# Performance work log

Measured on AMD Instinct MI355X. Metric: run time of the kernel, lower is better.

The kernel has to match this reference:

```python
import jax, jax.numpy as jnp
import numpy as np

EMBED = 1024
HEADS = 16
HEAD_DIM = EMBED // HEADS
N, SEQ = 4, 2048


def setup_inputs() -> dict:
    key = jax.random.key(0)
    ks = jax.random.split(key, 9)
    values = jax.random.normal(ks[0], (N, SEQ, EMBED), dtype=jnp.float32)
    keys = jax.random.normal(ks[1], (N, SEQ, EMBED), dtype=jnp.float32)
    query = jax.random.normal(ks[2], (N, SEQ, EMBED), dtype=jnp.float32)
    mask = jax.random.randint(ks[3], (N, 1, SEQ, SEQ), 0, 2, dtype=jnp.int32)
    s_h = 1.0 / np.sqrt(HEAD_DIM)
    s_e = 1.0 / np.sqrt(EMBED)
    Wv = jax.random.normal(ks[4], (HEAD_DIM, HEAD_DIM), dtype=jnp.float32) * s_h
    Wk = jax.random.normal(ks[5], (HEAD_DIM, HEAD_DIM), dtype=jnp.float32) * s_h
    Wq = jax.random.normal(ks[6], (HEAD_DIM, HEAD_DIM), dtype=jnp.float32) * s_h
    Wo = jax.random.normal(ks[7], (EMBED, EMBED), dtype=jnp.float32) * s_e
    bo = jax.random.normal(ks[8], (EMBED,), dtype=jnp.float32) * 0.01
    return {"values": values, "keys": keys, "query": query, "mask": mask,
            "Wv": Wv, "Wk": Wk, "Wq": Wq, "Wo": Wo, "bo": bo}


def reference(values, keys, query, mask, Wv, Wk, Wq, Wo, bo):
    n, q_len = query.shape[0], query.shape[1]
    k_len, v_len = keys.shape[1], values.shape[1]
    # split heads: [N, L, H, D]
    v = values.reshape(n, v_len, HEADS, HEAD_DIM)
    k = keys.reshape(n, k_len, HEADS, HEAD_DIM)
    q = query.reshape(n, q_len, HEADS, HEAD_DIM)
    # per-head linear projections (nn.Linear: x @ W.T)
    v = jnp.einsum('nlhd,ed->nlhe', v, Wv)
    k = jnp.einsum('nlhd,ed->nlhe', k, Wk)
    q = jnp.einsum('nlhd,ed->nlhe', q, Wq)
    # [N, H, Q, K] scores
    energy = jnp.einsum('nqhd,nkhd->nhqk', q, k)
    energy = jnp.where(mask == 0, jnp.float32(-1e20), energy)
    # note: original scales by sqrt(embed_size), not sqrt(head_dim)
    attention = jax.nn.softmax(energy / jnp.sqrt(jnp.float32(EMBED)), axis=3)
    out = jnp.einsum('nhql,nlhd->nqhd', attention, v).reshape(n, q_len, EMBED)
    return out @ Wo.T + bo
```

## Files before the change

kernel.cpp:

```cpp
#include <hip/hip_runtime.h>
#include <hip/hip_bf16.h>

typedef __attribute__((ext_vector_type(8))) short bfx8;
typedef __attribute__((ext_vector_type(4))) float fx4;
typedef __attribute__((ext_vector_type(16))) float f32x16;
typedef __attribute__((ext_vector_type(4))) unsigned u32x4;

#define MFMA16(a,b,c) __builtin_amdgcn_mfma_f32_16x16x32_bf16((a),(b),(c),0,0,0)
#define MFMA32(a,b,c) __builtin_amdgcn_mfma_f32_32x32x16_bf16((a),(b),(c),0,0,0)

__device__ __forceinline__ unsigned short bfc(float x){
  return __builtin_bit_cast(unsigned short, __float2bfloat16(x));
}
__device__ __forceinline__ unsigned pack2(float a, float b){
  return (unsigned)bfc(a) | ((unsigned)bfc(b) << 16);
}
__device__ __forceinline__ bfx8 cvt8(const float* p){
  const float4* q = (const float4*)p;
  float4 a = q[0], b = q[1];
  bfx8 r;
  r[0]=(short)bfc(a.x); r[1]=(short)bfc(a.y); r[2]=(short)bfc(a.z); r[3]=(short)bfc(a.w);
  r[4]=(short)bfc(b.x); r[5]=(short)bfc(b.y); r[6]=(short)bfc(b.z); r[7]=(short)bfc(b.w);
  return r;
}
__device__ __forceinline__ void g2l16(const void* g, void* l){
  __builtin_amdgcn_global_load_lds((const __attribute__((address_space(1))) unsigned*)g,
                                   (__attribute__((address_space(3))) unsigned*)l, 16, 0, 0);
}
__device__ __forceinline__ float mexp(float zv, unsigned mws, int pos){
  float e = __builtin_amdgcn_exp2f(zv);
  unsigned msk = (unsigned)(((int)(mws << (31-pos))) >> 31);
  return __builtin_bit_cast(float, __builtin_bit_cast(unsigned, e) & msk);
}
__device__ __forceinline__ f32x16 zero16(){
  f32x16 z;
  #pragma unroll
  for (int i=0;i<16;++i) z[i] = 0.f;
  return z;
}

#define SCL 0.04508422002778f

__global__ __launch_bounds__(256) void prep_k(const float* __restrict__ Xv, const float* __restrict__ Xk,
                                              const float* __restrict__ Xq,
                                              const float* __restrict__ Wv, const float* __restrict__ Wk,
                                              const float* __restrict__ Wq,
                                              const int* __restrict__ M, const float* __restrict__ Wo,
                                              unsigned short* __restrict__ Vt, unsigned short* __restrict__ Kb,
                                              unsigned short* __restrict__ Qb,
                                              unsigned long long* __restrict__ mT,
                                              unsigned short* __restrict__ Wob){
  int bid = blockIdx.x;
  int tid = threadIdx.x, l = tid & 63, wv = tid >> 6, g = l >> 4, j = l & 15;
  if (bid >= 3072){
    int pid = bid - 3072;
    if (pid < 1024){
      int task = pid*4 + wv;
      int n = task >> 10, rem = task & 1023, kt = rem >> 5, qc = rem & 31;
      int qbase = qc*64;
      const int* mp = M + (size_t)n*2048*2048 + (size_t)kt*64 + l;
      unsigned long long myw = 0;
      for (int qq = 0; qq < 64; ++qq){
        unsigned long long b = __ballot(mp[(size_t)(qbase+qq)*2048] != 0);
        if (l == qq) myw = b;
      }
      mT[((size_t)n*32 + kt)*2048 + qbase + l] = myw;
    } else {
      int i = ((pid-1024)*256 + tid)*8;
      bfx8 v = cvt8(Wo + i);
      *(bfx8*)(Wob + i) = v;
    }
    return;
  }
  int which = bid >> 10;
  int r = bid & 1023;
  int nh = r >> 4, sb = r & 15;
  int n = nh >> 4, h = nh & 15;
  const float* X = (which==0) ? Xv : ((which==1) ? Xk : Xq);
  const float* W = (which==0) ? Wv : ((which==1) ? Wk : Wq);
  int s0 = sb*128 + wv*32;
  size_t xbase = (size_t)n*2048*1024 + (size_t)h*64;

  if (which){
    float sc = (which==2) ? SCL : 1.0f;
    bfx8 bw[4][2];
    for (int nt=0;nt<4;++nt) for (int ks=0;ks<2;++ks)
      bw[nt][ks] = cvt8(W + (nt*16 + j)*64 + ks*32 + g*8);
    bfx8 ax[2][2];
    for (int mt=0;mt<2;++mt){
      const float* xp = X + xbase + (size_t)(s0 + mt*16 + j)*1024;
      for (int ks=0;ks<2;++ks) ax[mt][ks] = cvt8(xp + ks*32 + g*8);
    }
    fx4 acc[2][4];
    for (int mt=0;mt<2;++mt) for (int nt=0;nt<4;++nt) acc[mt][nt] = (fx4){0.f,0.f,0.f,0.f};
    for (int mt=0;mt<2;++mt) for (int nt=0;nt<4;++nt) for (int ks=0;ks<2;++ks)
      acc[mt][nt] = MFMA16(ax[mt][ks], bw[nt][ks], acc[mt][nt]);
    unsigned short* O = ((which==1) ? Kb : Qb) + (size_t)nh*2048*64;
    for (int mt=0;mt<2;++mt) for (int nt=0;nt<4;++nt) for (int rr=0;rr<4;++rr){
      int s = s0 + mt*16 + g*4 + rr, e = nt*16 + j;
      O[(size_t)s*64 + e] = bfc(acc[mt][nt][rr]*sc);
    }
  } else {
    bfx8 aw[4][2];
    for (int mt=0;mt<4;++mt) for (int ks=0;ks<2;++ks)
      aw[mt][ks] = cvt8(W + (mt*16 + j)*64 + ks*32 + g*8);
    bfx8 bx[2][2];
    for (int nt=0;nt<2;++nt){
      const float* xp = X + xbase + (size_t)(s0 + nt*16 + j)*1024;
      for (int ks=0;ks<2;++ks) bx[nt][ks] = cvt8(xp + ks*32 + g*8);
    }
    fx4 acc[4][2];
    for (int mt=0;mt<4;++mt) for (int nt=0;nt<2;++nt) acc[mt][nt] = (fx4){0.f,0.f,0.f,0.f};
    for (int mt=0;mt<4;++mt) for (int nt=0;nt<2;++nt) for (int ks=0;ks<2;++ks)
      acc[mt][nt] = MFMA16(aw[mt][ks], bx[nt][ks], acc[mt][nt]);
    unsigned short* O = Vt + (size_t)nh*64*2048;
    for (int mt=0;mt<4;++mt) for (int nt=0;nt<2;++nt) for (int rr=0;rr<4;++rr){
      int d = mt*16 + g*4 + rr, s = s0 + nt*16 + j;
      O[(size_t)d*2048 + s] = bfc(acc[mt][nt][rr]);
    }
  }
}

__global__ __launch_bounds__(512, 4) void flash_k(const unsigned short* __restrict__ Qb,
                                                  const unsigned short* __restrict__ Kb,
                                                  const unsigned short* __restrict__ Vt,
                                                  const unsigned long long* __restrict__ mT,
                                                  unsigned short* __restrict__ AO){
  __shared__ short lK[2][64*64];
  __shared__ short lV[2][64*64];
  int tid = threadIdx.x;
  int l = tid & 63, wv = tid >> 6, hi = l >> 5, c = l & 31;
  int cl7 = c & 7, hi4 = hi*4;
  int bid = blockIdx.x;
  int nh = bid >> 3, qb = bid & 7;
  int n = nh >> 4, h = nh & 15;
  const unsigned short* Qp = Qb + (size_t)nh*131072;
  const unsigned short* Kp = Kb + (size_t)nh*131072;
  const unsigned short* Vp = Vt + (size_t)nh*131072;
  int q = qb*256 + wv*32 + c;
  bfx8 qf[4];
  #pragma unroll
  for (int s=0;s<4;++s) qf[s] = *(const bfx8*)(Qp + (size_t)q*64 + s*16 + hi*8);
  f32x16 accO0 = zero16(), accO1 = zero16();
  float ls = 0.f;
  const unsigned long long* mrow = mT + (size_t)n*65536 + q;
  int rowK0 = c*128;
  int rowK1 = rowK0 + 4096;

  int sidx = wv*64 + l;
  int srow = sidx >> 3, scs = (sidx & 7) ^ (srow & 7);
  const unsigned short* Ksrc = Kp + (size_t)srow*64 + scs*8;
  const unsigned short* Vsrc = Vp + (size_t)srow*2048 + scs*8;

  g2l16(Ksrc, (char*)lK[0] + sidx*16);
  g2l16(Vsrc, (char*)lV[0] + sidx*16);
  __syncthreads();

#define PROC_TILE(zz, mws, TT, VB) do { \
    unsigned Wt[8]; \
    _Pragma("unroll") \
    for (int wi=0; wi<8; ++wi){ \
      const int r0 = 2*wi; \
      const int pos = (r0&3) + 8*(r0>>2); \
      float p0_ = mexp((zz)[r0],   (mws), pos); \
      float p1_ = mexp((zz)[r0+1], (mws), pos+1); \
      ls += p0_ + p1_; \
      Wt[wi] = pack2(p0_, p1_); \
    } \
    _Pragma("unroll") \
    for (int mm=0; mm<2; ++mm){ \
      unsigned xa = hi ? Wt[4*mm+0] : Wt[4*mm+2]; \
      unsigned xb = hi ? Wt[4*mm+1] : Wt[4*mm+3]; \
      unsigned ra = (unsigned)__shfl_xor((int)xa, 32); \
      unsigned rb = (unsigned)__shfl_xor((int)xb, 32); \
      u32x4 pw; \
      pw.x = hi ? ra : Wt[4*mm+0]; \
      pw.y = hi ? rb : Wt[4*mm+1]; \
      pw.z = hi ? Wt[4*mm+2] : ra; \
      pw.w = hi ? Wt[4*mm+3] : rb; \
      bfx8 pb = __builtin_bit_cast(bfx8, pw); \
      const int ch2 = 2*((TT)*2+mm); \
      bfx8 vf0 = *(const bfx8*)((VB) + rowK0 + (((ch2+hi) ^ cl7) << 4)); \
      bfx8 vf1 = *(const bfx8*)((VB) + rowK1 + (((ch2+hi) ^ cl7) << 4)); \
      accO0 = MFMA32(vf0, pb, accO0); \
      accO1 = MFMA32(vf1, pb, accO1); \
    } \
  } while(0)

#define ATTN_ITER(BUF, NBUF, kt) do { \
    if ((kt) < 31){ \
      g2l16(Ksrc + (size_t)((kt)+1)*4096, (char*)lK[NBUF] + sidx*16); \
      g2l16(Vsrc + (size_t)((kt)+1)*64,   (char*)lV[NBUF] + sidx*16); \
    } \
    unsigned long long mw = mrow[(size_t)(kt)*2048]; \
    const char* KB = (const char*)lK[BUF]; \
    const char* VB = (const char*)lV[BUF]; \
    f32x16 z0 = zero16(), z1 = zero16(); \
    _Pragma("unroll") \
    for (int s=0; s<4; ++s){ \
      bfx8 kf0 = *(const bfx8*)(KB + rowK0 + (((2*s+hi) ^ cl7) << 4)); \
      bfx8 kf1 = *(const bfx8*)(KB + rowK1 + (((2*s+hi) ^ cl7) << 4)); \
      z0 = MFMA32(kf0, qf[s], z0); \
      z1 = MFMA32(kf1, qf[s], z1); \
    } \
    unsigned mws0 = ((unsigned)mw) >> hi4; \
    unsigned mws1 = ((unsigned)(mw >> 32)) >> hi4; \
    PROC_TILE(z0, mws0, 0, VB); \
    PROC_TILE(z1, mws1, 1, VB); \
    __syncthreads(); \
  } while(0)

  #pragma unroll 1
  for (int kt2 = 0; kt2 < 32; kt2 += 2){
    ATTN_ITER(0, 1, kt2);
    ATTN_ITER(1, 0, kt2+1);
  }
#undef ATTN_ITER
#undef PROC_TILE

  ls += __shfl_xor(ls, 32);
  float inv = 1.0f / ls;
  unsigned short* aop = AO + ((size_t)n*2048 + q)*1024 + h*64;
  #pragma unroll
  for (int u=0; u<4; ++u){
    int d0 = u*8 + hi4;
    ushort4 o;
    o.x = bfc(accO0[4*u+0]*inv); o.y = bfc(accO0[4*u+1]*inv);
    o.z = bfc(accO0[4*u+2]*inv); o.w = bfc(accO0[4*u+3]*inv);
    *(ushort4*)(aop + d0) = o;
    ushort4 o1;
    o1.x = bfc(accO1[4*u+0]*inv); o1.y = bfc(accO1[4*u+1]*inv);
    o1.z = bfc(accO1[4*u+2]*inv); o1.w = bfc(accO1[4*u+3]*inv);
    *(ushort4*)(aop + 32 + d0) = o1;
  }
}

__global__ __launch_bounds__(256) void gemm_k(const unsigned short* __restrict__ AO,
                                              const unsigned short* __restrict__ Wob,
                                              const float* __restrict__ bo, float* __restrict__ out){
  __shared__ short lA[2][128*32], lB[2][128*32];
  int tid = threadIdx.x, l = tid & 63, wv = tid >> 6, g = l >> 4, j = l & 15;
  int wr = wv >> 1, wc = wv & 1;
  int bid = blockIdx.x;
  int m0 = (bid >> 3)*128, n0 = (bid & 7)*128;
  fx4 acc[4][4];
  #pragma unroll
  for (int mt=0;mt<4;++mt) for (int nt=0;nt<4;++nt) acc[mt][nt] = (fx4){0.f,0.f,0.f,0.f};

  int sbase = wv*128;
  int sidx0 = sbase + l, sidx1 = sbase + 64 + l;
  int srow0 = sidx0 >> 2, sc0 = sidx0 & 3;
  int srow1 = sidx1 >> 2, sc1 = sidx1 & 3;
  const unsigned short* Asrc0 = AO  + (size_t)(m0+srow0)*1024 + sc0*8;
  const unsigned short* Asrc1 = AO  + (size_t)(m0+srow1)*1024 + sc1*8;
  const unsigned short* Bsrc0 = Wob + (size_t)(n0+srow0)*1024 + sc0*8;
  const unsigned short* Bsrc1 = Wob + (size_t)(n0+srow1)*1024 + sc1*8;

  #define GSTAGE(b, kb) do { \
    g2l16(Asrc0 + (kb)*32, (char*)lA[b] + sidx0*16); \
    g2l16(Asrc1 + (kb)*32, (char*)lA[b] + sidx1*16); \
    g2l16(Bsrc0 + (kb)*32, (char*)lB[b] + sidx0*16); \
    g2l16(Bsrc1 + (kb)*32, (char*)lB[b] + sidx1*16); \
  } while(0)

  GSTAGE(0, 0);
  __syncthreads();
  int b = 0;
  for (int kb = 0; kb < 32; ++kb){
    if (kb < 31) GSTAGE(b^1, kb+1);
    bfx8 af[4], bfr[4];
    #pragma unroll
    for (int mt=0;mt<4;++mt) af[mt]  = *(const bfx8*)((const char*)lA[b] + (wr*64 + mt*16 + j)*64 + g*16);
    #pragma unroll
    for (int nt=0;nt<4;++nt) bfr[nt] = *(const bfx8*)((const char*)lB[b] + (wc*64 + nt*16 + j)*64 + g*16);
    #pragma unroll
    for (int mt=0;mt<4;++mt)
      #pragma unroll
      for (int nt=0;nt<4;++nt)
        acc[mt][nt] = MFMA16(af[mt], bfr[nt], acc[mt][nt]);
    __syncthreads();
    b ^= 1;
  }
  #undef GSTAGE

  #pragma unroll
  for (int mt=0;mt<4;++mt)
    #pragma unroll
    for (int nt=0;nt<4;++nt){
      int mm = m0 + wr*64 + mt*16 + g*4;
      int oo = n0 + wc*64 + nt*16 + j;
      float bb = bo[oo];
      #pragma unroll
      for (int rr=0;rr<4;++rr)
        out[(size_t)(mm+rr)*1024 + oo] = acc[mt][nt][rr] + bb;
    }
}

extern "C" void kernel_launch(void* const* d_in, const int* in_sizes, int n_in,
                              void* d_out, int out_size, void* d_ws, size_t ws_size,
                              hipStream_t stream){
  const float* V  = (const float*)d_in[0];
  const float* K  = (const float*)d_in[1];
  const float* Q  = (const float*)d_in[2];
  const int*   M  = (const int*)d_in[3];
  const float* Wv = (const float*)d_in[4];
  const float* Wk = (const float*)d_in[5];
  const float* Wq = (const float*)d_in[6];
  const float* Wo = (const float*)d_in[7];
  const float* bo = (const float*)d_in[8];

  char* ws = (char*)d_ws;
  unsigned short* Qb = (unsigned short*)(ws + ((size_t)0  << 20));
  unsigned short* Kb = (unsigned short*)(ws + ((size_t)16 << 20));
  unsigned short* Vt = (unsigned short*)(ws + ((size_t)32 << 20));
  unsigned short* AO = (unsigned short*)(ws + ((size_t)48 << 20));
  unsigned long long* mT = (unsigned long long*)(ws + ((size_t)64 << 20));
  unsigned short* Wob = (unsigned short*)(ws + ((size_t)66 << 20));

  hipLaunchKernelGGL(prep_k,  dim3(4608), dim3(256), 0, stream,
                     V, K, Q, Wv, Wk, Wq, M, Wo, Vt, Kb, Qb, mT, Wob);
  hipLaunchKernelGGL(flash_k, dim3(512),  dim3(512), 0, stream, Qb, Kb, Vt, mT, AO);
  hipLaunchKernelGGL(gemm_k,  dim3(512),  dim3(256), 0, stream, AO, Wob, bo, (float*)d_out);
}
```

Baseline: 192.8 us.

## Use 32x32x8 MFMA for PV to drop shuffles; smaller blocks, remapped grid

The PV product now uses the 32x32x8 bf16 MFMA, so each lane's packed P values feed the B operand directly and the cross-half __shfl_xor exchange goes away. The attention kernel also changes from 512 threads covering 256 queries to 256 threads covering 128 queries per block, with twice as many blocks and a blockIdx remap that interleaves heads. Each thread now stages two 16-byte chunks per tile, the LDS XOR swizzle gains a second term to cut bank conflicts, and the mask word is prefetched one tile ahead. In exchange, PV issues twice as many MFMAs at half the K depth, and K/V tiles are loaded into LDS by twice as many blocks.

```diff
diff --git a/kernel.cpp b/kernel.cpp
--- a/kernel.cpp
+++ b/kernel.cpp
@@ -2,12 +2,21 @@
 #include <hip/hip_bf16.h>
 
 typedef __attribute__((ext_vector_type(8))) short bfx8;
+typedef __attribute__((ext_vector_type(4))) short bfx4;
 typedef __attribute__((ext_vector_type(4))) float fx4;
 typedef __attribute__((ext_vector_type(16))) float f32x16;
-typedef __attribute__((ext_vector_type(4))) unsigned u32x4;
 
 #define MFMA16(a,b,c) __builtin_amdgcn_mfma_f32_16x16x32_bf16((a),(b),(c),0,0,0)
 #define MFMA32(a,b,c) __builtin_amdgcn_mfma_f32_32x32x16_bf16((a),(b),(c),0,0,0)
+
+__device__ __forceinline__ f32x16 mfma32x8(bfx4 a, bfx4 b, f32x16 c){
+#if __has_builtin(__builtin_amdgcn_mfma_f32_32x32x8bf16_1k)
+  return __builtin_amdgcn_mfma_f32_32x32x8bf16_1k(a, b, c, 0, 0, 0);
+#else
+  asm("v_mfma_f32_32x32x8_bf16 %0, %1, %2, %0" : "+v"(c) : "v"(a), "v"(b));
+  return c;
+#endif
+}
 
 __device__ __forceinline__ unsigned short bfc(float x){
   return __builtin_bit_cast(unsigned short, __float2bfloat16(x));
@@ -121,7 +130,7 @@
   }
 }
 
-__global__ __launch_bounds__(512, 4) void flash_k(const unsigned short* __restrict__ Qb,
+__global__ __launch_bounds__(256, 4) void flash_k(const unsigned short* __restrict__ Qb,
                                                   const unsigned short* __restrict__ Kb,
                                                   const unsigned short* __restrict__ Vt,
                                                   const unsigned long long* __restrict__ mT,
@@ -130,14 +139,16 @@
   __shared__ short lV[2][64*64];
   int tid = threadIdx.x;
   int l = tid & 63, wv = tid >> 6, hi = l >> 5, c = l & 31;
-  int cl7 = c & 7, hi4 = hi*4;
-  int bid = blockIdx.x;
-  int nh = bid >> 3, qb = bid & 7;
+  int swc = (c & 7) ^ ((c >> 3) & 3);
+  int hi4 = hi*4;
+  int bid0 = blockIdx.x;
+  int bid = (bid0 & 7)*128 + (bid0 >> 3);
+  int nh = bid >> 4, qb = bid & 15;
   int n = nh >> 4, h = nh & 15;
   const unsigned short* Qp = Qb + (size_t)nh*131072;
   const unsigned short* Kp = Kb + (size_t)nh*131072;
   const unsigned short* Vp = Vt + (size_t)nh*131072;
-  int q = qb*256 + wv*32 + c;
+  int q = qb*128 + wv*32 + c;
   bfx8 qf[4];
   #pragma unroll
   for (int s=0;s<4;++s) qf[s] = *(const bfx8*)(Qp + (size_t)q*64 + s*16 + hi*8);
@@ -147,14 +158,24 @@
   int rowK0 = c*128;
   int rowK1 = rowK0 + 4096;
 
-  int sidx = wv*64 + l;
-  int srow = sidx >> 3, scs = (sidx & 7) ^ (srow & 7);
-  const unsigned short* Ksrc = Kp + (size_t)srow*64 + scs*8;
-  const unsigned short* Vsrc = Vp + (size_t)srow*2048 + scs*8;
-
-  g2l16(Ksrc, (char*)lK[0] + sidx*16);
-  g2l16(Vsrc, (char*)lV[0] + sidx*16);
+  int sidx0 = wv*64 + l, sidx1 = sidx0 + 256;
+  int srow0 = sidx0 >> 3, scs0 = (sidx0 & 7) ^ (srow0 & 7) ^ ((srow0 >> 3) & 3);
+  int srow1 = sidx1 >> 3, scs1 = (sidx1 & 7) ^ (srow1 & 7) ^ ((srow1 >> 3) & 3);
+  const unsigned short* Ksrc0 = Kp + (size_t)srow0*64 + scs0*8;
+  const unsigned short* Ksrc1 = Kp + (size_t)srow1*64 + scs1*8;
+  const unsigned short* Vsrc0 = Vp + (size_t)srow0*2048 + scs0*8;
+  const unsigned short* Vsrc1 = Vp + (size_t)srow1*2048 + scs1*8;
+
+  #define STAGE(b, kt) do { \
+    g2l16(Ksrc0 + (size_t)(kt)*4096, (char*)lK[b] + sidx0*16); \
+    g2l16(Ksrc1 + (size_t)(kt)*4096, (char*)lK[b] + sidx1*16); \
+    g2l16(Vsrc0 + (size_t)(kt)*64,   (char*)lV[b] + sidx0*16); \
+    g2l16(Vsrc1 + (size_t)(kt)*64,   (char*)lV[b] + sidx1*16); \
+  } while(0)
+
+  STAGE(0, 0);
   __syncthreads();
+  unsigned long long mwcur = mrow[0];
 
 #define PROC_TILE(zz, mws, TT, VB) do { \
     unsigned Wt[8]; \
@@ -168,38 +189,28 @@
       Wt[wi] = pack2(p0_, p1_); \
     } \
     _Pragma("unroll") \
-    for (int mm=0; mm<2; ++mm){ \
-      unsigned xa = hi ? Wt[4*mm+0] : Wt[4*mm+2]; \
-      unsigned xb = hi ? Wt[4*mm+1] : Wt[4*mm+3]; \
-      unsigned ra = (unsigned)__shfl_xor((int)xa, 32); \
-      unsigned rb = (unsigned)__shfl_xor((int)xb, 32); \
-      u32x4 pw; \
-      pw.x = hi ? ra : Wt[4*mm+0]; \
-      pw.y = hi ? rb : Wt[4*mm+1]; \
-      pw.z = hi ? Wt[4*mm+2] : ra; \
-      pw.w = hi ? Wt[4*mm+3] : rb; \
-      bfx8 pb = __builtin_bit_cast(bfx8, pw); \
-      const int ch2 = 2*((TT)*2+mm); \
-      bfx8 vf0 = *(const bfx8*)((VB) + rowK0 + (((ch2+hi) ^ cl7) << 4)); \
-      bfx8 vf1 = *(const bfx8*)((VB) + rowK1 + (((ch2+hi) ^ cl7) << 4)); \
-      accO0 = MFMA32(vf0, pb, accO0); \
-      accO1 = MFMA32(vf1, pb, accO1); \
+    for (int wl=0; wl<4; ++wl){ \
+      const int w = 4*(TT) + wl; \
+      uint2 u2; u2.x = Wt[2*wl]; u2.y = Wt[2*wl+1]; \
+      bfx4 pb = __builtin_bit_cast(bfx4, u2); \
+      bfx4 vf0 = *(const bfx4*)((VB) + rowK0 + (((w ^ swc) << 4) + hi*8)); \
+      bfx4 vf1 = *(const bfx4*)((VB) + rowK1 + (((w ^ swc) << 4) + hi*8)); \
+      accO0 = mfma32x8(vf0, pb, accO0); \
+      accO1 = mfma32x8(vf1, pb, accO1); \
     } \
   } while(0)
 
 #define ATTN_ITER(BUF, NBUF, kt) do { \
-    if ((kt) < 31){ \
-      g2l16(Ksrc + (size_t)((kt)+1)*4096, (char*)lK[NBUF] + sidx*16); \
-      g2l16(Vsrc + (size_t)((kt)+1)*64,   (char*)lV[NBUF] + sidx*16); \
-    } \
-    unsigned long long mw = mrow[(size_t)(kt)*2048]; \
+    if ((kt) < 31) STAGE(NBUF, (kt)+1); \
+    unsigned long long mw = mwcur; \
+    mwcur = mrow[(size_t)((kt)+1 < 32 ? (kt)+1 : 31)*2048]; \
     const char* KB = (const char*)lK[BUF]; \
     const char* VB = (const char*)lV[BUF]; \
     f32x16 z0 = zero16(), z1 = zero16(); \
     _Pragma("unroll") \
     for (int s=0; s<4; ++s){ \
-      bfx8 kf0 = *(const bfx8*)(KB + rowK0 + (((2*s+hi) ^ cl7) << 4)); \
-      bfx8 kf1 = *(const bfx8*)(KB + rowK1 + (((2*s+hi) ^ cl7) << 4)); \
+      bfx8 kf0 = *(const bfx8*)(KB + rowK0 + (((2*s+hi) ^ swc) << 4)); \
+      bfx8 kf1 = *(const bfx8*)(KB + rowK1 + (((2*s+hi) ^ swc) << 4)); \
       z0 = MFMA32(kf0, qf[s], z0); \
       z1 = MFMA32(kf1, qf[s], z1); \
     } \
@@ -217,6 +228,7 @@
   }
 #undef ATTN_ITER
 #undef PROC_TILE
+#undef STAGE
 
   ls += __shfl_xor(ls, 32);
   float inv = 1.0f / ls;
@@ -319,6 +331,6 @@
 
   hipLaunchKernelGGL(prep_k,  dim3(4608), dim3(256), 0, stream,
                      V, K, Q, Wv, Wk, Wq, M, Wo, Vt, Kb, Qb, mT, Wob);
-  hipLaunchKernelGGL(flash_k, dim3(512),  dim3(512), 0, stream, Qb, Kb, Vt, mT, AO);
+  hipLaunchKernelGGL(flash_k, dim3(1024), dim3(256), 0, stream, Qb, Kb, Vt, mT, AO);
   hipLaunchKernelGGL(gemm_k,  dim3(512),  dim3(256), 0, stream, AO, Wob, bo, (float*)d_out);
 }
```

Measured after the change: 192.1 us. No clear change (-0.3%).
